# Kernel tuning notes

Hardware: AMD Instinct MI355X
Metric: run time of the kernel (lower is better)

## Reference

```python
import jax, jax.numpy as jnp
import numpy as np


def setup_inputs() -> dict:
    key = jax.random.key(0)
    k1, k2 = jax.random.split(key)
    N, M, D = 8192, 8192, 64
    X1 = jax.random.normal(k1, (N, D), dtype=jnp.float32)
    X2 = jax.random.normal(k2, (M, D), dtype=jnp.float32)
    l = jnp.float32(1.0)
    sigma_f = jnp.float32(1.0)
    return {"X1": X1, "X2": X2, "l": l, "sigma_f": sigma_f}


def reference(X1, X2, l, sigma_f):
    sq1 = jnp.sum(X1 * X1, axis=1)               # [N]
    sq2 = jnp.sum(X2 * X2, axis=1)               # [M]
    cross = jnp.einsum("nd,md->nm", X1, X2)      # [N,M] GEMM
    dist = sq1[:, None] + sq2[None, :] - 2.0 * cross
    dist = jnp.maximum(dist, 0.0)                # clamp numerical negatives
    return sigma_f ** 2 * jnp.exp(-0.5 * dist / l ** 2)
```

## Files before the change

kernel.cpp:

```cpp
#include <hip/hip_runtime.h>
#include <hip/hip_bf16.h>

#define DD 64
#define TN 64
#define TM 256

typedef short short8 __attribute__((ext_vector_type(8)));
typedef unsigned short us8 __attribute__((ext_vector_type(8)));
typedef float f32x4 __attribute__((ext_vector_type(4)));

__device__ __forceinline__ float bf2f(unsigned short h) {
    union { unsigned u; float f; } v; v.u = ((unsigned)h) << 16;
    return v.f;
}
__device__ __forceinline__ unsigned short f2bf(float x) {
    __hip_bfloat16 b = __float2bfloat16(x);
    unsigned short u;
    __builtin_memcpy(&u, &b, 2);
    return u;
}

__global__ __launch_bounds__(256, 2) void sqexp_kernel(
    const float* __restrict__ X1, const float* __restrict__ X2,
    const float* __restrict__ lp, const float* __restrict__ sfp,
    float* __restrict__ out, int N, int M)
{
    __shared__ __align__(16) unsigned char ldsbuf[TM * DD * 2 * 2];
    __shared__ float sq1[TN];
    __shared__ float sq2[TM];

    unsigned short* Bh = (unsigned short*)ldsbuf;
    unsigned short* Bl = (unsigned short*)(ldsbuf + 32768);

    const int t    = threadIdx.x;
    const int w    = t >> 6;
    const int lane = t & 63;
    const int n0   = blockIdx.y * TN;
    const int m0   = blockIdx.x * TM;

    const int wr = (w >> 1) * 32;
    const int wc = (w & 1) * 128;

    const float4* Bp = (const float4*)(X2 + (size_t)(m0 + t) * DD);
    float4 bv[16];
    #pragma unroll
    for (int j = 0; j < 16; ++j) bv[j] = Bp[j];

    short8 ah[2][2], al[2][2];
    float sqa[2];
    #pragma unroll
    for (int fm = 0; fm < 2; ++fm) {
        const int row = n0 + wr + fm * 16 + (lane & 15);
        const float4* Ap = (const float4*)(X1 + (size_t)row * DD) + (lane >> 4) * 2;
        float p = 0.0f;
        #pragma unroll
        for (int ks = 0; ks < 2; ++ks) {
            float4 f0 = Ap[ks * 8];
            float4 f1 = Ap[ks * 8 + 1];
            float xs[8] = { f0.x, f0.y, f0.z, f0.w, f1.x, f1.y, f1.z, f1.w };
            us8 hv, lv;
            #pragma unroll
            for (int e = 0; e < 8; ++e) {
                p = fmaf(xs[e], xs[e], p);
                unsigned short h = f2bf(xs[e]);
                hv[e] = h;
                lv[e] = f2bf(xs[e] - bf2f(h));
            }
            __builtin_memcpy(&ah[fm][ks], &hv, 16);
            __builtin_memcpy(&al[fm][ks], &lv, 16);
        }
        p += __shfl_xor(p, 16);
        p += __shfl_xor(p, 32);
        sqa[fm] = p;
    }

    {
        float s2 = 0.0f;
        #pragma unroll
        for (int j = 0; j < 16; ++j)
            s2 += fmaf(bv[j].x, bv[j].x, fmaf(bv[j].y, bv[j].y,
                  fmaf(bv[j].z, bv[j].z, bv[j].w * bv[j].w)));
        sq2[t] = s2;
        if ((w & 1) == 0 && (lane >> 4) == 0) {
            sq1[wr + 0 * 16 + lane] = sqa[0];
            sq1[wr + 1 * 16 + lane] = sqa[1];
        }
    }

    #pragma unroll
    for (int c = 0; c < 8; ++c) {
        float4 f0 = bv[2 * c], f1 = bv[2 * c + 1];
        float xs[8] = { f0.x, f0.y, f0.z, f0.w, f1.x, f1.y, f1.z, f1.w };
        us8 hv, lv;
        #pragma unroll
        for (int e = 0; e < 8; ++e) {
            unsigned short h = f2bf(xs[e]);
            hv[e] = h;
            lv[e] = f2bf(xs[e] - bf2f(h));
        }
        int byte = t * 128 + ((c * 16) ^ ((t & 7) << 4));
        *(us8*)&Bh[byte >> 1] = hv;
        *(us8*)&Bl[byte >> 1] = lv;
    }
    __syncthreads();

    f32x4 acc[2][8] = {};
    #pragma unroll
    for (int ks = 0; ks < 2; ++ks) {
        #pragma unroll
        for (int fn = 0; fn < 8; ++fn) {
            int brow = wc + fn * 16 + (lane & 15);
            int byte = brow * 128 + (((ks * 64) + (lane >> 4) * 16) ^ ((brow & 7) << 4));
            short8 bh = *(const short8*)&Bh[byte >> 1];
            short8 bl = *(const short8*)&Bl[byte >> 1];
            #pragma unroll
            for (int fm = 0; fm < 2; ++fm) {
                acc[fm][fn] = __builtin_amdgcn_mfma_f32_16x16x32_bf16(bh, ah[fm][ks], acc[fm][fn], 0, 0, 0);
                acc[fm][fn] = __builtin_amdgcn_mfma_f32_16x16x32_bf16(bl, ah[fm][ks], acc[fm][fn], 0, 0, 0);
                acc[fm][fn] = __builtin_amdgcn_mfma_f32_16x16x32_bf16(bh, al[fm][ks], acc[fm][fn], 0, 0, 0);
            }
        }
    }
    __syncthreads();

    const float lv_  = lp[0], sf = sfp[0];
    const float c1   = -0.5f / (lv_ * lv_);
    const float cm2  = -2.0f * c1;
    const float amp  = sf * sf;

    float a1[2];
    #pragma unroll
    for (int fm = 0; fm < 2; ++fm) a1[fm] = c1 * sq1[wr + fm * 16 + (lane & 15)];

    #pragma unroll
    for (int fn = 0; fn < 8; ++fn) {
        f32x4 s = *(const f32x4*)&sq2[wc + fn * 16 + (lane >> 4) * 4];
        f32x4 a2 = c1 * s;
        #pragma unroll
        for (int fm = 0; fm < 2; ++fm) {
            f32x4 o;
            #pragma unroll
            for (int r = 0; r < 4; ++r) {
                float arg = fminf(fmaf(cm2, acc[fm][fn][r], a1[fm] + a2[r]), 0.0f);
                o[r] = amp * __expf(arg);
            }
            int R = wr + fm * 16 + (lane & 15);
            int C = wc + fn * 16 + (lane >> 4) * 4;
            int byte = R * 1024 + ((C * 4) ^ ((R & 7) << 4));
            *(f32x4*)(ldsbuf + byte) = o;
        }
    }
    __syncthreads();

    #pragma unroll
    for (int i = 0; i < 16; ++i) {
        int R = w * 16 + i;
        f32x4 v = *(const f32x4*)(ldsbuf + R * 1024 + ((lane ^ (R & 7)) * 16));
        size_t off = (size_t)(n0 + R) * M + m0 + 4 * lane;
        *(f32x4*)&out[off] = v;
    }
}

extern "C" void kernel_launch(void* const* d_in, const int* in_sizes, int n_in,
                              void* d_out, int out_size, void* d_ws, size_t ws_size,
                              hipStream_t stream) {
    const float* X1 = (const float*)d_in[0];
    const float* X2 = (const float*)d_in[1];
    const float* lp = (const float*)d_in[2];
    const float* sf = (const float*)d_in[3];
    float* out = (float*)d_out;
    const int N = in_sizes[0] / DD;
    const int M = in_sizes[1] / DD;
    dim3 grid(M / TM, N / TN);
    sqexp_kernel<<<grid, 256, 0, stream>>>(X1, X2, lp, sf, out, N, M);
}
```

Baseline: 77.00 us.

## Split block's column tile into two halves and overlap store with next load

```diff
diff --git a/kernel.cpp b/kernel.cpp
--- a/kernel.cpp
+++ b/kernel.cpp
@@ -3,7 +3,7 @@
 
 #define DD 64
 #define TN 64
-#define TM 256
+#define TM 128
 
 typedef short short8 __attribute__((ext_vector_type(8)));
 typedef unsigned short us8 __attribute__((ext_vector_type(8)));
@@ -25,29 +25,109 @@
     const float* __restrict__ lp, const float* __restrict__ sfp,
     float* __restrict__ out, int N, int M)
 {
-    __shared__ __align__(16) unsigned char ldsbuf[TM * DD * 2 * 2];
+    __shared__ __align__(16) unsigned char Bbuf[2 * TM * DD * 2];
+    __shared__ __align__(16) unsigned char Obuf[TN * TM * 4];
     __shared__ float sq1[TN];
     __shared__ float sq2[TM];
 
-    unsigned short* Bh = (unsigned short*)ldsbuf;
-    unsigned short* Bl = (unsigned short*)(ldsbuf + 32768);
+    unsigned short* Bh = (unsigned short*)Bbuf;
+    unsigned short* Bl = (unsigned short*)(Bbuf + TM * DD * 2);
 
     const int t    = threadIdx.x;
     const int w    = t >> 6;
     const int lane = t & 63;
     const int n0   = blockIdx.y * TN;
-    const int m0   = blockIdx.x * TM;
+    const int m0   = blockIdx.x * (2 * TM);
 
     const int wr = (w >> 1) * 32;
-    const int wc = (w & 1) * 128;
+    const int wc = (w & 1) * 64;
 
-    const float4* Bp = (const float4*)(X2 + (size_t)(m0 + t) * DD);
-    float4 bv[16];
-    #pragma unroll
-    for (int j = 0; j < 16; ++j) bv[j] = Bp[j];
+    const float lv_ = lp[0], sf = sfp[0];
+    const float c1  = -0.5f / (lv_ * lv_);
+    const float cm2 = -2.0f * c1;
+    const float amp = sf * sf;
+
+    const int brow_ = t >> 1;
+    const int bhalf = t & 1;
+
+    auto loadB = [&](int mbase, float4 (&f)[8]) {
+        const float4* Bp = (const float4*)(X2 + (size_t)(mbase + brow_) * DD) + bhalf * 8;
+        #pragma unroll
+        for (int j = 0; j < 8; ++j) f[j] = Bp[j];
+    };
+    auto writeB = [&](float4 (&f)[8]) {
+        float s2 = 0.0f;
+        #pragma unroll
+        for (int c = 0; c < 4; ++c) {
+            float4 f0 = f[2 * c], f1 = f[2 * c + 1];
+            float xs[8] = { f0.x, f0.y, f0.z, f0.w, f1.x, f1.y, f1.z, f1.w };
+            us8 hv, lv;
+            #pragma unroll
+            for (int e = 0; e < 8; ++e) {
+                s2 = fmaf(xs[e], xs[e], s2);
+                unsigned short h = f2bf(xs[e]);
+                hv[e] = h;
+                lv[e] = f2bf(xs[e] - bf2f(h));
+            }
+            int byte = brow_ * 128 + (((bhalf * 4 + c) * 16) ^ ((brow_ & 7) << 4));
+            *(us8*)&Bh[byte >> 1] = hv;
+            *(us8*)&Bl[byte >> 1] = lv;
+        }
+        s2 += __shfl_xor(s2, 1);
+        if (bhalf == 0) sq2[brow_] = s2;
+    };
 
     short8 ah[2][2], al[2][2];
-    float sqa[2];
+    auto computeTile = [&](f32x4 (&acc)[2][4]) {
+        #pragma unroll
+        for (int ks = 0; ks < 2; ++ks) {
+            #pragma unroll
+            for (int fn = 0; fn < 4; ++fn) {
+                int br   = wc + fn * 16 + (lane & 15);
+                int byte = br * 128 + (((ks * 64) + (lane >> 4) * 16) ^ ((br & 7) << 4));
+                short8 bh = *(const short8*)&Bh[byte >> 1];
+                short8 bl = *(const short8*)&Bl[byte >> 1];
+                #pragma unroll
+                for (int fm = 0; fm < 2; ++fm) {
+                    acc[fm][fn] = __builtin_amdgcn_mfma_f32_16x16x32_bf16(bh, ah[fm][ks], acc[fm][fn], 0, 0, 0);
+                    acc[fm][fn] = __builtin_amdgcn_mfma_f32_16x16x32_bf16(bl, ah[fm][ks], acc[fm][fn], 0, 0, 0);
+                    acc[fm][fn] = __builtin_amdgcn_mfma_f32_16x16x32_bf16(bh, al[fm][ks], acc[fm][fn], 0, 0, 0);
+                }
+            }
+        }
+    };
+    auto epilogueTile = [&](f32x4 (&acc)[2][4]) {
+        float a1[2];
+        #pragma unroll
+        for (int fm = 0; fm < 2; ++fm) a1[fm] = c1 * sq1[wr + fm * 16 + (lane & 15)];
+        #pragma unroll
+        for (int fn = 0; fn < 4; ++fn) {
+            f32x4 s  = *(const f32x4*)&sq2[wc + fn * 16 + (lane >> 4) * 4];
+            f32x4 a2 = c1 * s;
+            #pragma unroll
+            for (int fm = 0; fm < 2; ++fm) {
+                f32x4 o;
+                #pragma unroll
+                for (int r = 0; r < 4; ++r) {
+                    float arg = fminf(fmaf(cm2, acc[fm][fn][r], a1[fm] + a2[r]), 0.0f);
+                    o[r] = amp * __expf(arg);
+                }
+                int R = wr + fm * 16 + (lane & 15);
+                int C = wc + fn * 16 + (lane >> 4) * 4;
+                *(f32x4*)(Obuf + R * 512 + ((C * 4) ^ ((R & 7) << 4))) = o;
+            }
+        }
+    };
+    auto storeTile = [&](int mbase) {
+        #pragma unroll
+        for (int i = 0; i < 8; ++i) {
+            int R = w * 16 + i * 2 + (lane >> 5);
+            int c = lane & 31;
+            f32x4 v = *(const f32x4*)(Obuf + R * 512 + ((c ^ (R & 7)) * 16));
+            *(f32x4*)&out[(size_t)(n0 + R) * M + mbase + 4 * c] = v;
+        }
+    };
+
     #pragma unroll
     for (int fm = 0; fm < 2; ++fm) {
         const int row = n0 + wr + fm * 16 + (lane & 15);
@@ -71,94 +151,35 @@
         }
         p += __shfl_xor(p, 16);
         p += __shfl_xor(p, 32);
-        sqa[fm] = p;
+        if ((w & 1) == 0 && (lane >> 4) == 0) sq1[wr + fm * 16 + lane] = p;
     }
 
     {
-        float s2 = 0.0f;
-        #pragma unroll
-        for (int j = 0; j < 16; ++j)
-            s2 += fmaf(bv[j].x, bv[j].x, fmaf(bv[j].y, bv[j].y,
-                  fmaf(bv[j].z, bv[j].z, bv[j].w * bv[j].w)));
-        sq2[t] = s2;
-        if ((w & 1) == 0 && (lane >> 4) == 0) {
-            sq1[wr + 0 * 16 + lane] = sqa[0];
-            sq1[wr + 1 * 16 + lane] = sqa[1];
-        }
-    }
-
-    #pragma unroll
-    for (int c = 0; c < 8; ++c) {
-        float4 f0 = bv[2 * c], f1 = bv[2 * c + 1];
-        float xs[8] = { f0.x, f0.y, f0.z, f0.w, f1.x, f1.y, f1.z, f1.w };
-        us8 hv, lv;
-        #pragma unroll
-        for (int e = 0; e < 8; ++e) {
-            unsigned short h = f2bf(xs[e]);
-            hv[e] = h;
-            lv[e] = f2bf(xs[e] - bf2f(h));
-        }
-        int byte = t * 128 + ((c * 16) ^ ((t & 7) << 4));
-        *(us8*)&Bh[byte >> 1] = hv;
-        *(us8*)&Bl[byte >> 1] = lv;
+        float4 f[8];
+        loadB(m0, f);
+        writeB(f);
     }
     __syncthreads();
 
-    f32x4 acc[2][8] = {};
-    #pragma unroll
-    for (int ks = 0; ks < 2; ++ks) {
-        #pragma unroll
-        for (int fn = 0; fn < 8; ++fn) {
-            int brow = wc + fn * 16 + (lane & 15);
-            int byte = brow * 128 + (((ks * 64) + (lane >> 4) * 16) ^ ((brow & 7) << 4));
-            short8 bh = *(const short8*)&Bh[byte >> 1];
-            short8 bl = *(const short8*)&Bl[byte >> 1];
-            #pragma unroll
-            for (int fm = 0; fm < 2; ++fm) {
-                acc[fm][fn] = __builtin_amdgcn_mfma_f32_16x16x32_bf16(bh, ah[fm][ks], acc[fm][fn], 0, 0, 0);
-                acc[fm][fn] = __builtin_amdgcn_mfma_f32_16x16x32_bf16(bl, ah[fm][ks], acc[fm][fn], 0, 0, 0);
-                acc[fm][fn] = __builtin_amdgcn_mfma_f32_16x16x32_bf16(bh, al[fm][ks], acc[fm][fn], 0, 0, 0);
-            }
-        }
+    f32x4 accA[2][4] = {};
+    computeTile(accA);
+    epilogueTile(accA);
+    __syncthreads();
+
+    {
+        float4 f[8];
+        loadB(m0 + TM, f);
+        storeTile(m0);
+        writeB(f);
     }
     __syncthreads();
 
-    const float lv_  = lp[0], sf = sfp[0];
-    const float c1   = -0.5f / (lv_ * lv_);
-    const float cm2  = -2.0f * c1;
-    const float amp  = sf * sf;
-
-    float a1[2];
-    #pragma unroll
-    for (int fm = 0; fm < 2; ++fm) a1[fm] = c1 * sq1[wr + fm * 16 + (lane & 15)];
-
-    #pragma unroll
-    for (int fn = 0; fn < 8; ++fn) {
-        f32x4 s = *(const f32x4*)&sq2[wc + fn * 16 + (lane >> 4) * 4];
-        f32x4 a2 = c1 * s;
-        #pragma unroll
-        for (int fm = 0; fm < 2; ++fm) {
-            f32x4 o;
-            #pragma unroll
-            for (int r = 0; r < 4; ++r) {
-                float arg = fminf(fmaf(cm2, acc[fm][fn][r], a1[fm] + a2[r]), 0.0f);
-                o[r] = amp * __expf(arg);
-            }
-            int R = wr + fm * 16 + (lane & 15);
-            int C = wc + fn * 16 + (lane >> 4) * 4;
-            int byte = R * 1024 + ((C * 4) ^ ((R & 7) << 4));
-            *(f32x4*)(ldsbuf + byte) = o;
-        }
-    }
+    f32x4 accB[2][4] = {};
+    computeTile(accB);
+    epilogueTile(accB);
     __syncthreads();
 
-    #pragma unroll
-    for (int i = 0; i < 16; ++i) {
-        int R = w * 16 + i;
-        f32x4 v = *(const f32x4*)(ldsbuf + R * 1024 + ((lane ^ (R & 7)) * 16));
-        size_t off = (size_t)(n0 + R) * M + m0 + 4 * lane;
-        *(f32x4*)&out[off] = v;
-    }
+    storeTile(m0 + TM);
 }
 
 extern "C" void kernel_launch(void* const* d_in, const int* in_sizes, int n_in,
@@ -171,6 +192,6 @@
     float* out = (float*)d_out;
     const int N = in_sizes[0] / DD;
     const int M = in_sizes[1] / DD;
-    dim3 grid(M / TM, N / TN);
+    dim3 grid(M / (2 * TM), N / TN);
     sqexp_kernel<<<grid, 256, 0, stream>>>(X1, X2, lp, sf, out, N, M);
 }
```

Result: slower. 82.11 us (+6.6%).
